# Performance work log

Hardware: AMD Instinct MI355X
Metric: run time of the kernel (lower is better)

The kernel has to match this reference:

```python
import jax, jax.numpy as jnp
import numpy as np

EPS = 1e-5

def gelu(x):
    return jax.nn.gelu(x, approximate=False)

def conv1x1(x, w, b):
    # x: [B,C,H,W], w: [O,C], b: [O]
    return jnp.einsum('bchw,oc->bohw', x, w) + b[None, :, None, None]

def dwconv3(x, w, b):
    # depthwise 3x3, w: [C,1,3,3]
    C = x.shape[1]
    y = jax.lax.conv_general_dilated(x, w, (1, 1), 'SAME',
                                     feature_group_count=C,
                                     dimension_numbers=('NCHW', 'OIHW', 'NCHW'))
    return y + b[None, :, None, None]

def groupnorm(x, g, b):
    # GroupNorm(1, C): normalize over (C,H,W) per sample, per-channel affine
    m = x.mean(axis=(1, 2, 3), keepdims=True)
    v = x.var(axis=(1, 2, 3), keepdims=True)
    xn = (x - m) * jax.lax.rsqrt(v + EPS)
    return xn * g[None, :, None, None] + b[None, :, None, None]

@jax.custom_vjp
def spike(u):
    return (u > 0.0).astype(u.dtype)

def _spike_fwd(u):
    return spike(u), u

def _spike_bwd(u, g):
    # rectangular surrogate gradient of width 0.5 around the threshold
    return (g * (jnp.abs(u) < 0.5).astype(g.dtype),)

spike.defvjp(_spike_fwd, _spike_bwd)

def lif_along(x, tau, vth, axis):
    # leaky-integrate-fire recurrence along `axis` (H or W) treated as time
    xt = jnp.moveaxis(x, axis, 0)  # [T, ...]
    z = jnp.zeros_like(xt[0])
    def step(carry, x_t):
        u_prev, o_prev = carry
        u = x_t + tau * u_prev * (1.0 - o_prev)  # hard reset on spike
        o = spike(u - vth)
        return (u, o), o
    _, out = jax.lax.scan(step, (z, z), xt)
    return jnp.moveaxis(out, 0, axis)


def setup_inputs() -> dict:
    key = jax.random.key(0)
    ks = jax.random.split(key, 8)
    B, C, H, W = 64, 96, 56, 56
    Hd = 4 * C
    def w(k, shape, s=0.02):
        return jax.random.normal(k, shape, jnp.float32) * s
    f32 = jnp.float32
    return dict(
        x=jax.random.normal(ks[0], (B, C, H, W), f32),
        n1g=jnp.ones(C, f32), n1b=jnp.zeros(C, f32),
        c1w=w(ks[1], (C, C)), c1b=jnp.zeros(C, f32),
        g1g=jnp.ones(C, f32), g1b=jnp.zeros(C, f32),
        dww=w(ks[2], (C, 1, 3, 3)), dwb=jnp.zeros(C, f32),
        g2g=jnp.ones(C, f32), g2b=jnp.zeros(C, f32),
        tau1=jnp.array(0.25, f32), vth1=jnp.array(-1.0, f32),
        tau2=jnp.array(0.25, f32), vth2=jnp.array(-1.0, f32),
        c21w=w(ks[3], (C, C)), c21b=jnp.zeros(C, f32),
        c22w=w(ks[4], (C, C)), c22b=jnp.zeros(C, f32),
        g3g=jnp.ones(C, f32), g3b=jnp.zeros(C, f32),
        c3w=w(ks[5], (C, C)), c3b=jnp.zeros(C, f32),
        n2g=jnp.ones(C, f32), n2b=jnp.zeros(C, f32),
        f1w=w(ks[6], (Hd, C)), f1b=jnp.zeros(Hd, f32),
        f2w=w(ks[7], (C, Hd)), f2b=jnp.zeros(C, f32),
    )


def reference(x, n1g, n1b, c1w, c1b, g1g, g1b, dww, dwb, g2g, g2b,
              tau1, vth1, tau2, vth2, c21w, c21b, c22w, c22b,
              g3g, g3b, c3w, c3b, n2g, n2b, f1w, f1b, f2w, f2b):
    shortcut = x
    # LIF module
    h = groupnorm(x, n1g, n1b)                               # block norm1 (MyNorm)
    h = gelu(groupnorm(conv1x1(h, c1w, c1b), g1g, g1b))      # conv1 -> norm1 -> GELU
    h = gelu(groupnorm(dwconv3(h, dww, dwb), g2g, g2b))      # dw1 -> norm2 -> GELU
    x_lr = lif_along(h, tau1, vth1, axis=2)                  # LIF over H
    x_td = lif_along(h, tau2, vth2, axis=3)                  # LIF over W
    h = gelu(conv1x1(x_lr, c21w, c21b)) + gelu(conv1x1(x_td, c22w, c22b))
    h = conv1x1(groupnorm(h, g3g, g3b), c3w, c3b)            # norm3 -> conv3
    x = shortcut + h
    # MLP branch (1x1 convs)
    m = groupnorm(x, n2g, n2b)
    m = conv1x1(gelu(conv1x1(m, f1w, f1b)), f2w, f2b)
    return x + m
```

## Files before the change

kernel.cpp:

```cpp
#include <hip/hip_runtime.h>

#define BB 64
#define CC 96
#define HH 56
#define WW 56
#define HWSZ (HH*WW)
#define CHW (CC*HWSZ)
#define NTOT ((size_t)BB*CHW)
#define S_SPLIT 32
#define CHUNK (CHW/S_SPLIT)
#define HD 384
#define NP 104

typedef float f32x4  __attribute__((ext_vector_type(4)));
typedef float f32x4v __attribute__((ext_vector_type(4)));
typedef short bf16x8 __attribute__((ext_vector_type(8)));
typedef unsigned short u16x4 __attribute__((ext_vector_type(4)));

__device__ __forceinline__ unsigned short f2bf(float f) {
    unsigned int u = __float_as_uint(f);
    u = (u + 0x7FFFu + ((u >> 16) & 1u)) >> 16;
    return (unsigned short)u;
}
__device__ __forceinline__ unsigned int cvtpk(float lo, float hi) {
    unsigned int r;
    asm("v_cvt_pk_bf16_f32 %0, %1, %2" : "=v"(r) : "v"(lo), "v"(hi));
    return r;
}
__device__ __forceinline__ unsigned short cvt1(float x) {
    return (unsigned short)cvtpk(x, x);
}
__device__ __forceinline__ float bf2f(unsigned short u) {
    return __uint_as_float(((unsigned int)u) << 16);
}
__device__ __forceinline__ float gelu_t(float x) {
    float s = x*x;
    float q = __builtin_fmaf(s, 0.102943f, 2.3021953f) * x;
    float t = exp2f(q);
    float r = __builtin_amdgcn_rcpf(1.0f + t);
    return __builtin_fmaf(-x, r, x);
}
__device__ __forceinline__ bf16x8 ldfrag(const unsigned short* p) {
    return *reinterpret_cast<const bf16x8*>(p);
}
template<int NPART>
__device__ __forceinline__ float2 stats_from_parts(const float2* __restrict__ part, int b) {
    int lane = threadIdx.x & 63;
    float s = 0.f, q = 0.f;
    for (int i = lane; i < NPART; i += 64) {
        float2 v = part[b*NPART + i];
        s += v.x; q += v.y;
    }
    #pragma unroll
    for (int off = 32; off > 0; off >>= 1) {
        s += __shfl_down(s, off);
        q += __shfl_down(q, off);
    }
    s = __shfl(s, 0); q = __shfl(q, 0);
    float mean = s / (float)CHW;
    float var  = q / (float)CHW - mean*mean;
    return make_float2(mean, rsqrtf(var + 1e-5f));
}

__global__ __launch_bounds__(256) void wconv(const float* __restrict__ c1w, const float* __restrict__ c21w,
        const float* __restrict__ c22w, const float* __restrict__ c3w,
        const float* __restrict__ f1w, const float* __restrict__ f2w,
        unsigned short* __restrict__ wbf) {
    int i = blockIdx.x*256 + threadIdx.x;
    int blk = i / 9216;
    int idx = i - blk*9216;
    int tm   = idx / 1536;
    int rem  = idx - tm*1536;
    int ks   = rem / 512;
    int rem2 = rem - ks*512;
    int lane = rem2 >> 3;
    int j    = rem2 & 7;
    int row = tm*16 + (lane & 15);
    int col = ks*32 + (lane >> 4)*8 + j;
    float v;
    if      (blk == 0) v = c1w [row*CC + col];
    else if (blk == 1) v = c21w[row*CC + col];
    else if (blk == 2) v = c22w[row*CC + col];
    else if (blk == 3) v = c3w [row*CC + col];
    else if (blk <  8) v = f1w[((blk-4)*CC + row)*CC + col];
    else               v = f2w[row*HD + (blk-8)*CC + col];
    wbf[i] = f2bf(v);
}

__global__ __launch_bounds__(256) void gn_partial(const float* __restrict__ in, float2* __restrict__ part) {
    int b = blockIdx.y, s = blockIdx.x;
    const float4* p = (const float4*)(in + (size_t)b*CHW + (size_t)s*CHUNK);
    float sum = 0.f, sq = 0.f;
    for (int i = threadIdx.x; i < CHUNK/4; i += 256) {
        float4 v = p[i];
        sum += v.x+v.y+v.z+v.w;
        sq  += v.x*v.x+v.y*v.y+v.z*v.z+v.w*v.w;
    }
    #pragma unroll
    for (int off = 32; off > 0; off >>= 1) {
        sum += __shfl_down(sum, off);
        sq  += __shfl_down(sq,  off);
    }
    __shared__ float2 red[4];
    int wid = threadIdx.x >> 6, lane = threadIdx.x & 63;
    if (lane == 0) red[wid] = make_float2(sum, sq);
    __syncthreads();
    if (threadIdx.x == 0) {
        for (int i = 1; i < 4; i++) { sum += red[i].x; sq += red[i].y; }
        part[b*S_SPLIT + s] = make_float2(sum, sq);
    }
}

template<bool IN_BF, bool OUT_RES, int NPART>
__global__ __launch_bounds__(256) void convk(const void* __restrict__ in_,
        const unsigned short* __restrict__ wbf, const float* __restrict__ bias,
        const float2* __restrict__ part_in, const float* __restrict__ gam, const float* __restrict__ bet,
        const float* __restrict__ res, void* __restrict__ out_, float2* __restrict__ part_out) {
    __shared__ unsigned short xs[128][NP];
    __shared__ float af0[CC], bf0[CC], af1[CC], bf1[CC];
    __shared__ float2 red[4];
    int tid = threadIdx.x;
    int b0 = blockIdx.y, b1 = b0 + 32;
    int hw0 = blockIdx.x * 64;
    int lane = tid & 63, wv = tid >> 6;
    int mh = wv >> 1, cg = wv & 1;
    bf16x8 wfr[9];
    {
        const unsigned short* wl = wbf + mh*4608 + lane*8;
        #pragma unroll
        for (int i = 0; i < 9; i++) wfr[i] = ldfrag(wl + i*512);
    }
    float2 st0 = stats_from_parts<NPART>(part_in, b0);
    float2 st1 = stats_from_parts<NPART>(part_in, b1);
    if (tid < CC) {
        float a0 = st0.y * gam[tid];
        af0[tid] = a0; bf0[tid] = __builtin_fmaf(-st0.x, a0, bet[tid]);
        float a1 = st1.y * gam[tid];
        af1[tid] = a1; bf1[tid] = __builtin_fmaf(-st1.x, a1, bet[tid]);
    }
    __syncthreads();
    {
        int colq = (tid & 15) * 4;
        for (int c4 = (tid >> 4)*4; c4 < CC; c4 += 64) {
            float v0[4][4], v1[4][4];
            #pragma unroll
            for (int j = 0; j < 4; j++) {
                int c = c4 + j;
                size_t off0 = (size_t)b0*CHW + (size_t)c*HWSZ + hw0 + colq;
                size_t off1 = (size_t)b1*CHW + (size_t)c*HWSZ + hw0 + colq;
                if (IN_BF) {
                    u16x4 u0 = *reinterpret_cast<const u16x4*>((const unsigned short*)in_ + off0);
                    u16x4 u1 = *reinterpret_cast<const u16x4*>((const unsigned short*)in_ + off1);
                    #pragma unroll
                    for (int jj = 0; jj < 4; jj++) {
                        v0[j][jj] = __builtin_fmaf(bf2f((unsigned short)u0[jj]), af0[c], bf0[c]);
                        v1[j][jj] = __builtin_fmaf(bf2f((unsigned short)u1[jj]), af1[c], bf1[c]);
                    }
                } else {
                    f32x4v f0 = *reinterpret_cast<const f32x4v*>((const float*)in_ + off0);
                    f32x4v f1 = *reinterpret_cast<const f32x4v*>((const float*)in_ + off1);
                    #pragma unroll
                    for (int jj = 0; jj < 4; jj++) {
                        v0[j][jj] = __builtin_fmaf(f0[jj], af0[c], bf0[c]);
                        v1[j][jj] = __builtin_fmaf(f1[jj], af1[c], bf1[c]);
                    }
                }
            }
            #pragma unroll
            for (int jj = 0; jj < 4; jj++) {
                *reinterpret_cast<uint2*>(&xs[colq+jj][c4]) =
                    make_uint2(cvtpk(v0[0][jj],v0[1][jj]), cvtpk(v0[2][jj],v0[3][jj]));
                *reinterpret_cast<uint2*>(&xs[64+colq+jj][c4]) =
                    make_uint2(cvtpk(v1[0][jj],v1[1][jj]), cvtpk(v1[2][jj],v1[3][jj]));
            }
        }
    }
    __syncthreads();
    int ln = lane & 15, k0 = (lane >> 4)*8, r0i = (lane >> 4)*4;
    f32x4 acc[3][4];
    #pragma unroll
    for (int t = 0; t < 3; t++)
        #pragma unroll
        for (int x = 0; x < 4; x++) acc[t][x] = (f32x4){0,0,0,0};
    __builtin_amdgcn_s_setprio(1);
    #pragma unroll
    for (int ks = 0; ks < 3; ks++) {
        bf16x8 bfr[4];
        #pragma unroll
        for (int xr = 0; xr < 4; xr++) bfr[xr] = ldfrag(&xs[cg*64 + xr*16 + ln][ks*32+k0]);
        #pragma unroll
        for (int tm = 0; tm < 3; tm++) {
            #pragma unroll
            for (int xr = 0; xr < 4; xr++)
                acc[tm][xr] = __builtin_amdgcn_mfma_f32_16x16x32_bf16(wfr[tm*3+ks], bfr[xr], acc[tm][xr], 0, 0, 0);
        }
    }
    __builtin_amdgcn_s_setprio(0);
    size_t obase = (size_t)(cg ? b1 : b0)*CHW + hw0;
    float s = 0.f, q = 0.f;
    #pragma unroll
    for (int tm = 0; tm < 3; tm++) {
        #pragma unroll
        for (int xr = 0; xr < 4; xr++) {
            #pragma unroll
            for (int r = 0; r < 4; r++) {
                int o = mh*48 + tm*16 + r0i + r;
                size_t idx = obase + (size_t)o*HWSZ + xr*16 + ln;
                float v = acc[tm][xr][r] + bias[o];
                if (OUT_RES) { v += res[idx]; ((float*)out_)[idx] = v; }
                else         { ((unsigned short*)out_)[idx] = cvt1(v); }
                s += v; q += v*v;
            }
        }
    }
    #pragma unroll
    for (int off = 32; off > 0; off >>= 1) { s += __shfl_down(s, off); q += __shfl_down(q, off); }
    if (lane == 0) red[wv] = make_float2(s, q);
    __syncthreads();
    if (tid == 0) {
        part_out[b0*49 + blockIdx.x] = make_float2(red[0].x + red[2].x, red[0].y + red[2].y);
        part_out[b1*49 + blockIdx.x] = make_float2(red[1].x + red[3].x, red[1].y + red[3].y);
    }
}

__global__ __launch_bounds__(256) void dw_fused(const unsigned short* __restrict__ t1,
        const float* __restrict__ dww, const float* __restrict__ dwb,
        const float2* __restrict__ part_in, const float* __restrict__ gam, const float* __restrict__ bet,
        unsigned short* __restrict__ t2, float2* __restrict__ part_out) {
    __shared__ float tile[HH*57];
    __shared__ float2 red[4];
    int bc = blockIdx.x;
    int b = bc / CC, c = bc - b*CC;
    int tid = threadIdx.x;
    float2 st = stats_from_parts<49>(part_in, b);
    float ga = gam[c]*st.y;
    float bb = __builtin_fmaf(-st.x, ga, bet[c]);
    const unsigned short* ip = t1 + (size_t)bc*HWSZ;
    for (int i = tid; i < HWSZ/4; i += 256) {
        u16x4 v = *reinterpret_cast<const u16x4*>(ip + (size_t)i*4);
        int h = i / 14;
        int w0 = (i - h*14)*4;
        float* tp = &tile[h*57 + w0];
        #pragma unroll
        for (int j = 0; j < 4; j++)
            tp[j] = gelu_t(__builtin_fmaf(bf2f((unsigned short)v[j]), ga, bb));
    }
    __syncthreads();
    float w00=dww[c*9+0],w01=dww[c*9+1],w02=dww[c*9+2],
          w10=dww[c*9+3],w11=dww[c*9+4],w12=dww[c*9+5],
          w20=dww[c*9+6],w21=dww[c*9+7],w22=dww[c*9+8];
    float bs = dwb[c];
    unsigned short* op = t2 + (size_t)bc*HWSZ;
    float s = 0.f, q = 0.f;
    for (int i = tid; i < HWSZ; i += 256) {
        int h = i/WW, w_ = i - h*WW;
        float acc = bs;
        int up = h > 0, dn = h < HH-1, lf = w_ > 0, rt = w_ < WW-1;
        const float* rm = &tile[(h-1)*57 + w_];
        const float* r0p = &tile[h*57 + w_];
        const float* rp = &tile[(h+1)*57 + w_];
        if (up) { if (lf) acc += rm[-1]*w00; acc += rm[0]*w01; if (rt) acc += rm[1]*w02; }
        if (lf) acc += r0p[-1]*w10;
        acc += r0p[0]*w11;
        if (rt) acc += r0p[1]*w12;
        if (dn) { if (lf) acc += rp[-1]*w20; acc += rp[0]*w21; if (rt) acc += rp[1]*w22; }
        op[i] = cvt1(acc);
        s += acc; q += acc*acc;
    }
    #pragma unroll
    for (int off = 32; off > 0; off >>= 1) { s += __shfl_down(s, off); q += __shfl_down(q, off); }
    int wid = tid >> 6, lane = tid & 63;
    if (lane == 0) red[wid] = make_float2(s, q);
    __syncthreads();
    if (tid == 0) {
        for (int i = 1; i < 4; i++) { s += red[i].x; q += red[i].y; }
        part_out[bc] = make_float2(s, q);
    }
}

__global__ __launch_bounds__(64) void lif_hw(const unsigned short* __restrict__ t2,
        unsigned char* __restrict__ xlr, unsigned char* __restrict__ xtd,
        const float2* __restrict__ part_in, const float* __restrict__ gam, const float* __restrict__ bet,
        const float* __restrict__ tau1p, const float* __restrict__ vth1p,
        const float* __restrict__ tau2p, const float* __restrict__ vth2p) {
    __shared__ unsigned short tile[HH*58];
    __shared__ unsigned char spA[HH*60];
    int bc = blockIdx.x;
    int b = bc / CC, c = bc - b*CC;
    int tid = threadIdx.x;
    float2 st = stats_from_parts<96>(part_in, b);
    float ga = gam[c]*st.y;
    float bb = __builtin_fmaf(-st.x, ga, bet[c]);
    const unsigned short* ip = t2 + (size_t)bc*HWSZ;
    for (int i = tid; i < HWSZ/4; i += 64) {
        u16x4 v = *reinterpret_cast<const u16x4*>(ip + i*4);
        int h = i / 14;
        int w0 = (i - h*14)*4;
        unsigned short* tp = &tile[h*58 + w0];
        #pragma unroll
        for (int j = 0; j < 4; j++)
            tp[j] = cvt1(gelu_t(__builtin_fmaf(bf2f((unsigned short)v[j]), ga, bb)));
    }
    __syncthreads();
    const float tau1 = *tau1p, vth1 = *vth1p;
    if (tid < WW) {
        float u = 0.f, o = 0.f;
        for (int h = 0; h < HH; h++) {
            float xv = bf2f(tile[h*58 + tid]);
            u = xv + tau1*u*(1.f - o);
            o = (u - vth1 > 0.f) ? 1.f : 0.f;
            spA[h*60 + tid] = (o != 0.f) ? 1 : 0;
        }
    }
    __syncthreads();
    const float tau2 = *tau2p, vth2 = *vth2p;
    if (tid < HH) {
        float u = 0.f, o = 0.f;
        int off = tid*58;
        for (int w_ = 0; w_ < WW; w_++) {
            float xv = bf2f(tile[off + w_]);
            u = xv + tau2*u*(1.f - o);
            o = (u - vth2 > 0.f) ? 1.f : 0.f;
            tile[off + w_] = (o != 0.f) ? 1 : 0;
        }
    }
    __syncthreads();
    size_t base = (size_t)bc*HWSZ;
    unsigned int* lr32 = (unsigned int*)(xlr + base);
    unsigned int* td32 = (unsigned int*)(xtd + base);
    for (int i = tid; i < HWSZ/4; i += 64) {
        int h = i / 14;
        int w0 = (i - h*14)*4;
        unsigned int a = (unsigned int)spA[h*60+w0] | ((unsigned int)spA[h*60+w0+1]<<8)
                       | ((unsigned int)spA[h*60+w0+2]<<16) | ((unsigned int)spA[h*60+w0+3]<<24);
        unsigned int t = (unsigned int)(tile[h*58+w0]&1) | ((unsigned int)(tile[h*58+w0+1]&1)<<8)
                       | ((unsigned int)(tile[h*58+w0+2]&1)<<16) | ((unsigned int)(tile[h*58+w0+3]&1)<<24);
        lr32[i] = a;
        td32[i] = t;
    }
}

__global__ __launch_bounds__(256) void dual_mfma(const unsigned char* __restrict__ xa_g, const unsigned char* __restrict__ xb_g,
        const unsigned short* __restrict__ w1bf, const float* __restrict__ b1,
        const unsigned short* __restrict__ w2bf, const float* __restrict__ b2,
        unsigned short* __restrict__ out, float2* __restrict__ part_out) {
    __shared__ unsigned short xa[64][NP];
    __shared__ unsigned short xb[64][NP];
    __shared__ float2 red[4];
    int tid = threadIdx.x;
    int b = blockIdx.y;
    int hw0 = blockIdx.x * 64;
    {
        int colq = (tid & 15) * 4;
        const unsigned char* ap = xa_g + (size_t)b*CHW + hw0 + colq;
        const unsigned char* bp = xb_g + (size_t)b*CHW + hw0 + colq;
        for (int c4 = (tid >> 4)*4; c4 < CC; c4 += 64) {
            unsigned int ua[4], ub[4];
            #pragma unroll
            for (int j = 0; j < 4; j++) {
                ua[j] = *reinterpret_cast<const unsigned int*>(ap + (size_t)(c4+j)*HWSZ);
                ub[j] = *reinterpret_cast<const unsigned int*>(bp + (size_t)(c4+j)*HWSZ);
            }
            #pragma unroll
            for (int jj = 0; jj < 4; jj++) {
                unsigned int sh = jj*8;
                unsigned int la = (((ua[0]>>sh)&1u)*0x3F80u) | (((ua[1]>>sh)&1u)*0x3F800000u);
                unsigned int ha = (((ua[2]>>sh)&1u)*0x3F80u) | (((ua[3]>>sh)&1u)*0x3F800000u);
                unsigned int lb = (((ub[0]>>sh)&1u)*0x3F80u) | (((ub[1]>>sh)&1u)*0x3F800000u);
                unsigned int hb = (((ub[2]>>sh)&1u)*0x3F80u) | (((ub[3]>>sh)&1u)*0x3F800000u);
                *reinterpret_cast<uint2*>(&xa[colq+jj][c4]) = make_uint2(la, ha);
                *reinterpret_cast<uint2*>(&xb[colq+jj][c4]) = make_uint2(lb, hb);
            }
        }
    }
    __syncthreads();
    int lane = tid & 63, wv = tid >> 6;
    int mh = wv >> 1, cg = wv & 1;
    int ln = lane & 15, k0 = (lane >> 4)*8, r0i = (lane >> 4)*4;
    const unsigned short* wl1 = w1bf + mh*4608 + lane*8;
    const unsigned short* wl2 = w2bf + mh*4608 + lane*8;
    f32x4 acc1[3][2], acc2[3][2];
    #pragma unroll
    for (int t = 0; t < 3; t++) {
        acc1[t][0] = (f32x4){0,0,0,0}; acc1[t][1] = (f32x4){0,0,0,0};
        acc2[t][0] = (f32x4){0,0,0,0}; acc2[t][1] = (f32x4){0,0,0,0};
    }
    __builtin_amdgcn_s_setprio(1);
    #pragma unroll
    for (int ks = 0; ks < 3; ks++) {
        bf16x8 bfa0 = ldfrag(&xa[cg*32 + ln][ks*32+k0]);
        bf16x8 bfa1 = ldfrag(&xa[cg*32 + 16 + ln][ks*32+k0]);
        bf16x8 bfb0 = ldfrag(&xb[cg*32 + ln][ks*32+k0]);
        bf16x8 bfb1 = ldfrag(&xb[cg*32 + 16 + ln][ks*32+k0]);
        #pragma unroll
        for (int tm = 0; tm < 3; tm++) {
            bf16x8 af1 = ldfrag(wl1 + (tm*3+ks)*512);
            bf16x8 af2 = ldfrag(wl2 + (tm*3+ks)*512);
            acc1[tm][0] = __builtin_amdgcn_mfma_f32_16x16x32_bf16(af1, bfa0, acc1[tm][0], 0, 0, 0);
            acc1[tm][1] = __builtin_amdgcn_mfma_f32_16x16x32_bf16(af1, bfa1, acc1[tm][1], 0, 0, 0);
            acc2[tm][0] = __builtin_amdgcn_mfma_f32_16x16x32_bf16(af2, bfb0, acc2[tm][0], 0, 0, 0);
            acc2[tm][1] = __builtin_amdgcn_mfma_f32_16x16x32_bf16(af2, bfb1, acc2[tm][1], 0, 0, 0);
        }
    }
    __builtin_amdgcn_s_setprio(0);
    size_t ob = (size_t)b*CHW + hw0;
    float s = 0.f, q = 0.f;
    #pragma unroll
    for (int tm = 0; tm < 3; tm++) {
        #pragma unroll
        for (int xr = 0; xr < 2; xr++) {
            #pragma unroll
            for (int r = 0; r < 4; r++) {
                int o = mh*48 + tm*16 + r0i + r;
                float v = gelu_t(acc1[tm][xr][r] + b1[o]) + gelu_t(acc2[tm][xr][r] + b2[o]);
                out[ob + (size_t)o*HWSZ + cg*32 + xr*16 + ln] = cvt1(v);
                s += v; q += v*v;
            }
        }
    }
    #pragma unroll
    for (int off = 32; off > 0; off >>= 1) { s += __shfl_down(s, off); q += __shfl_down(q, off); }
    if (lane == 0) red[wv] = make_float2(s, q);
    __syncthreads();
    if (tid == 0) {
        for (int i = 1; i < 4; i++) { s += red[i].x; q += red[i].y; }
        part_out[b*49 + blockIdx.x] = make_float2(s, q);
    }
}

__global__ __launch_bounds__(256, 6) void mlp_mfma(float* __restrict__ xio, const float2* __restrict__ part_in,
        const float* __restrict__ gam, const float* __restrict__ bet,
        const unsigned short* __restrict__ wbf, const float* __restrict__ b1, const float* __restrict__ b2) {
    __shared__ unsigned short xs[64][NP];
    __shared__ unsigned short mc[64][NP];
    __shared__ float afc[CC], bfc[CC];
    int tid = threadIdx.x;
    int b = blockIdx.y;
    int hw0 = blockIdx.x * 64;
    int lane = tid & 63, wv = tid >> 6;
    int mh = wv >> 1;
    int cg = wv & 1;
    float2 st = stats_from_parts<49>(part_in, b);
    if (tid < CC) {
        float a = st.y * gam[tid];
        afc[tid] = a; bfc[tid] = __builtin_fmaf(-st.x, a, bet[tid]);
    }
    __syncthreads();
    {
        int col = tid & 63;
        size_t base = (size_t)b*CHW + hw0 + col;
        for (int c4 = (tid >> 6)*4; c4 < CC; c4 += 16) {
            float v[4];
            #pragma unroll
            for (int j = 0; j < 4; j++) {
                int c = c4 + j;
                float rv = xio[base + (size_t)c*HWSZ];
                v[j] = __builtin_fmaf(rv, afc[c], bfc[c]);
            }
            *reinterpret_cast<uint2*>(&xs[col][c4]) =
                make_uint2(cvtpk(v[0],v[1]), cvtpk(v[2],v[3]));
        }
    }
    __syncthreads();
    int ln = lane & 15, k0 = (lane >> 4)*8;
    int r0i = (lane >> 4)*4;
    int xrow0 = cg*32 + ln;
    int xrow1 = xrow0 + 16;
    f32x4 ao[3][2];
    #pragma unroll
    for (int t = 0; t < 3; t++) { ao[t][0] = (f32x4){0,0,0,0}; ao[t][1] = (f32x4){0,0,0,0}; }
    for (int ch = 0; ch < 4; ch++) {
        const unsigned short* w1l = wbf + (4+ch)*9216 + mh*4608 + lane*8;
        const unsigned short* w2l = wbf + (8+ch)*9216 + mh*4608 + lane*8;
        f32x4 c1[3][2];
        #pragma unroll
        for (int t = 0; t < 3; t++) { c1[t][0] = (f32x4){0,0,0,0}; c1[t][1] = (f32x4){0,0,0,0}; }
        __builtin_amdgcn_s_setprio(1);
        #pragma unroll
        for (int ks = 0; ks < 3; ks++) {
            bf16x8 bfa = ldfrag(&xs[xrow0][ks*32+k0]);
            bf16x8 bfb = ldfrag(&xs[xrow1][ks*32+k0]);
            #pragma unroll
            for (int tm = 0; tm < 3; tm++) {
                bf16x8 af = ldfrag(w1l + (tm*3+ks)*512);
                c1[tm][0] = __builtin_amdgcn_mfma_f32_16x16x32_bf16(af, bfa, c1[tm][0], 0, 0, 0);
                c1[tm][1] = __builtin_amdgcn_mfma_f32_16x16x32_bf16(af, bfb, c1[tm][1], 0, 0, 0);
            }
        }
        __builtin_amdgcn_s_setprio(0);
        #pragma unroll
        for (int tm = 0; tm < 3; tm++) {
            int d0 = mh*48 + tm*16 + r0i;
            int dch = ch*CC + d0;
            float g0 = gelu_t(c1[tm][0][0] + b1[dch+0]);
            float g1 = gelu_t(c1[tm][0][1] + b1[dch+1]);
            float g2 = gelu_t(c1[tm][0][2] + b1[dch+2]);
            float g3 = gelu_t(c1[tm][0][3] + b1[dch+3]);
            *reinterpret_cast<uint2*>(&mc[xrow0][d0]) = make_uint2(cvtpk(g0,g1), cvtpk(g2,g3));
            float h0 = gelu_t(c1[tm][1][0] + b1[dch+0]);
            float h1 = gelu_t(c1[tm][1][1] + b1[dch+1]);
            float h2 = gelu_t(c1[tm][1][2] + b1[dch+2]);
            float h3 = gelu_t(c1[tm][1][3] + b1[dch+3]);
            *reinterpret_cast<uint2*>(&mc[xrow1][d0]) = make_uint2(cvtpk(h0,h1), cvtpk(h2,h3));
        }
        __syncthreads();
        __builtin_amdgcn_s_setprio(1);
        #pragma unroll
        for (int ks = 0; ks < 3; ks++) {
            bf16x8 bfa = ldfrag(&mc[xrow0][ks*32+k0]);
            bf16x8 bfb = ldfrag(&mc[xrow1][ks*32+k0]);
            #pragma unroll
            for (int tm = 0; tm < 3; tm++) {
                bf16x8 af = ldfrag(w2l + (tm*3+ks)*512);
                ao[tm][0] = __builtin_amdgcn_mfma_f32_16x16x32_bf16(af, bfa, ao[tm][0], 0, 0, 0);
                ao[tm][1] = __builtin_amdgcn_mfma_f32_16x16x32_bf16(af, bfb, ao[tm][1], 0, 0, 0);
            }
        }
        __builtin_amdgcn_s_setprio(0);
        __syncthreads();
    }
    size_t ob = (size_t)b*CHW + hw0 + cg*32 + ln;
    #pragma unroll
    for (int tm = 0; tm < 3; tm++) {
        #pragma unroll
        for (int r = 0; r < 4; r++) {
            int o = mh*48 + tm*16 + r0i + r;
            size_t i0 = ob + (size_t)o*HWSZ;
            float bo = b2[o];
            xio[i0]      = xio[i0]      + bo + ao[tm][0][r];
            xio[i0 + 16] = xio[i0 + 16] + bo + ao[tm][1][r];
        }
    }
}

extern "C" void kernel_launch(void* const* d_in, const int* in_sizes, int n_in,
                              void* d_out, int out_size, void* d_ws, size_t ws_size,
                              hipStream_t stream) {
    (void)in_sizes; (void)n_in; (void)out_size; (void)ws_size;
    const float* x    = (const float*)d_in[0];
    const float* n1g  = (const float*)d_in[1];
    const float* n1b  = (const float*)d_in[2];
    const float* c1w  = (const float*)d_in[3];
    const float* c1b  = (const float*)d_in[4];
    const float* g1g  = (const float*)d_in[5];
    const float* g1b  = (const float*)d_in[6];
    const float* dww  = (const float*)d_in[7];
    const float* dwb  = (const float*)d_in[8];
    const float* g2g  = (const float*)d_in[9];
    const float* g2b  = (const float*)d_in[10];
    const float* tau1 = (const float*)d_in[11];
    const float* vth1 = (const float*)d_in[12];
    const float* tau2 = (const float*)d_in[13];
    const float* vth2 = (const float*)d_in[14];
    const float* c21w = (const float*)d_in[15];
    const float* c21b = (const float*)d_in[16];
    const float* c22w = (const float*)d_in[17];
    const float* c22b = (const float*)d_in[18];
    const float* g3g  = (const float*)d_in[19];
    const float* g3b  = (const float*)d_in[20];
    const float* c3w  = (const float*)d_in[21];
    const float* c3b  = (const float*)d_in[22];
    const float* n2g  = (const float*)d_in[23];
    const float* n2b  = (const float*)d_in[24];
    const float* f1w  = (const float*)d_in[25];
    const float* f1b  = (const float*)d_in[26];
    const float* f2w  = (const float*)d_in[27];
    const float* f2b  = (const float*)d_in[28];
    float* out = (float*)d_out;

    unsigned short* A   = (unsigned short*)d_ws;
    unsigned short* Bb  = A  + NTOT;
    unsigned short* Cc  = Bb + NTOT;
    unsigned short* WBF = Cc + NTOT;
    float2* part0 = (float2*)(WBF + 110592);
    float2* part1 = part0 + 64*32;
    float2* part2 = part1 + 64*49;
    float2* part3 = part2 + 64*96;
    float2* part4 = part3 + 64*49;

    const unsigned short* Wc1  = WBF;
    const unsigned short* Wc21 = WBF + 9216;
    const unsigned short* Wc22 = WBF + 18432;
    const unsigned short* Wc3  = WBF + 27648;

    unsigned char* Au8 = (unsigned char*)A;
    unsigned char* Cu8 = (unsigned char*)Cc;

    dim3 gStat(S_SPLIT, BB);
    dim3 gPair(HWSZ/64, BB/2);
    dim3 gSing(HWSZ/64, BB);

    wconv<<<432,256,0,stream>>>(c1w, c21w, c22w, c3w, f1w, f2w, WBF);
    gn_partial<<<gStat,256,0,stream>>>(x, part0);
    convk<false,false,S_SPLIT><<<gPair,256,0,stream>>>(x, Wc1, c1b, part0, n1g, n1b, nullptr, A, part1);
    dw_fused<<<BB*CC,256,0,stream>>>(A, dww, dwb, part1, g1g, g1b, Bb, part2);
    lif_hw<<<BB*CC,64,0,stream>>>(Bb, Au8, Cu8, part2, g2g, g2b, tau1, vth1, tau2, vth2);
    dual_mfma<<<gSing,256,0,stream>>>(Au8, Cu8, Wc21, c21b, Wc22, c22b, Bb, part3);
    convk<true,true,49><<<gPair,256,0,stream>>>(Bb, Wc3, c3b, part3, g3g, g3b, x, out, part4);
    mlp_mfma<<<gSing,256,0,stream>>>(out, part4, n2g, n2b, WBF, f1b, f2b);
}
```

Measured before the change: 270.6 us.

## Run H and W LIF scans concurrently and pack two planes per block

The LIF kernel now processes two (b,c) planes per 256-thread block. Within each plane, one wavefront runs the H-direction scan while another runs the W-direction scan at the same time, instead of running them one after the other. The W-scan output goes to a separate spike buffer rather than overwriting the input tile. The goal is to shorten the serial recurrence critical path and raise occupancy, at the cost of more shared memory per block.

```diff
diff --git a/kernel.cpp b/kernel.cpp
--- a/kernel.cpp
+++ b/kernel.cpp
@@ -278,63 +278,76 @@
     }
 }
 
-__global__ __launch_bounds__(64) void lif_hw(const unsigned short* __restrict__ t2,
+__global__ __launch_bounds__(256) void lif_hw(const unsigned short* __restrict__ t2,
         unsigned char* __restrict__ xlr, unsigned char* __restrict__ xtd,
         const float2* __restrict__ part_in, const float* __restrict__ gam, const float* __restrict__ bet,
         const float* __restrict__ tau1p, const float* __restrict__ vth1p,
         const float* __restrict__ tau2p, const float* __restrict__ vth2p) {
-    __shared__ unsigned short tile[HH*58];
-    __shared__ unsigned char spA[HH*60];
-    int bc = blockIdx.x;
+    __shared__ unsigned short tile[2][HH*58];
+    __shared__ unsigned char  spA[2][HH*60];
+    __shared__ unsigned char  spB[2][HH*60];
+    int tid = threadIdx.x;
+    int pl = tid >> 7;
+    int lt = tid & 127;
+    int bc = blockIdx.x*2 + pl;
     int b = bc / CC, c = bc - b*CC;
-    int tid = threadIdx.x;
     float2 st = stats_from_parts<96>(part_in, b);
     float ga = gam[c]*st.y;
     float bb = __builtin_fmaf(-st.x, ga, bet[c]);
     const unsigned short* ip = t2 + (size_t)bc*HWSZ;
-    for (int i = tid; i < HWSZ/4; i += 64) {
-        u16x4 v = *reinterpret_cast<const u16x4*>(ip + i*4);
+    for (int i = lt; i < HWSZ/4; i += 128) {
+        u16x4 v = *reinterpret_cast<const u16x4*>(ip + (size_t)i*4);
         int h = i / 14;
         int w0 = (i - h*14)*4;
-        unsigned short* tp = &tile[h*58 + w0];
+        unsigned short* tp = &tile[pl][h*58 + w0];
         #pragma unroll
         for (int j = 0; j < 4; j++)
             tp[j] = cvt1(gelu_t(__builtin_fmaf(bf2f((unsigned short)v[j]), ga, bb)));
     }
     __syncthreads();
-    const float tau1 = *tau1p, vth1 = *vth1p;
-    if (tid < WW) {
-        float u = 0.f, o = 0.f;
-        for (int h = 0; h < HH; h++) {
-            float xv = bf2f(tile[h*58 + tid]);
-            u = xv + tau1*u*(1.f - o);
-            o = (u - vth1 > 0.f) ? 1.f : 0.f;
-            spA[h*60 + tid] = (o != 0.f) ? 1 : 0;
-        }
-    }
-    __syncthreads();
-    const float tau2 = *tau2p, vth2 = *vth2p;
-    if (tid < HH) {
-        float u = 0.f, o = 0.f;
-        int off = tid*58;
-        for (int w_ = 0; w_ < WW; w_++) {
-            float xv = bf2f(tile[off + w_]);
-            u = xv + tau2*u*(1.f - o);
-            o = (u - vth2 > 0.f) ? 1.f : 0.f;
-            tile[off + w_] = (o != 0.f) ? 1 : 0;
+    {
+        int role = (tid >> 6) & 1;
+        int lane = tid & 63;
+        if (role == 0) {
+            const float tau1 = *tau1p, vth1 = *vth1p;
+            if (lane < WW) {
+                float u = 0.f, o = 0.f;
+                #pragma unroll 4
+                for (int h = 0; h < HH; h++) {
+                    float xv = bf2f(tile[pl][h*58 + lane]);
+                    u = xv + tau1*u*(1.f - o);
+                    o = (u - vth1 > 0.f) ? 1.f : 0.f;
+                    spA[pl][h*60 + lane] = (o != 0.f) ? 1 : 0;
+                }
+            }
+        } else {
+            const float tau2 = *tau2p, vth2 = *vth2p;
+            if (lane < HH) {
+                float u = 0.f, o = 0.f;
+                int off = lane*58;
+                #pragma unroll 4
+                for (int w_ = 0; w_ < WW; w_++) {
+                    float xv = bf2f(tile[pl][off + w_]);
+                    u = xv + tau2*u*(1.f - o);
+                    o = (u - vth2 > 0.f) ? 1.f : 0.f;
+                    spB[pl][lane*60 + w_] = (o != 0.f) ? 1 : 0;
+                }
+            }
         }
     }
     __syncthreads();
     size_t base = (size_t)bc*HWSZ;
     unsigned int* lr32 = (unsigned int*)(xlr + base);
     unsigned int* td32 = (unsigned int*)(xtd + base);
-    for (int i = tid; i < HWSZ/4; i += 64) {
+    for (int i = lt; i < HWSZ/4; i += 128) {
         int h = i / 14;
         int w0 = (i - h*14)*4;
-        unsigned int a = (unsigned int)spA[h*60+w0] | ((unsigned int)spA[h*60+w0+1]<<8)
-                       | ((unsigned int)spA[h*60+w0+2]<<16) | ((unsigned int)spA[h*60+w0+3]<<24);
-        unsigned int t = (unsigned int)(tile[h*58+w0]&1) | ((unsigned int)(tile[h*58+w0+1]&1)<<8)
-                       | ((unsigned int)(tile[h*58+w0+2]&1)<<16) | ((unsigned int)(tile[h*58+w0+3]&1)<<24);
+        const unsigned char* pa = &spA[pl][h*60 + w0];
+        const unsigned char* pb = &spB[pl][h*60 + w0];
+        unsigned int a = (unsigned int)pa[0] | ((unsigned int)pa[1]<<8)
+                       | ((unsigned int)pa[2]<<16) | ((unsigned int)pa[3]<<24);
+        unsigned int t = (unsigned int)pb[0] | ((unsigned int)pb[1]<<8)
+                       | ((unsigned int)pb[2]<<16) | ((unsigned int)pb[3]<<24);
         lr32[i] = a;
         td32[i] = t;
     }
@@ -594,7 +607,7 @@
     gn_partial<<<gStat,256,0,stream>>>(x, part0);
     convk<false,false,S_SPLIT><<<gPair,256,0,stream>>>(x, Wc1, c1b, part0, n1g, n1b, nullptr, A, part1);
     dw_fused<<<BB*CC,256,0,stream>>>(A, dww, dwb, part1, g1g, g1b, Bb, part2);
-    lif_hw<<<BB*CC,64,0,stream>>>(Bb, Au8, Cu8, part2, g2g, g2b, tau1, vth1, tau2, vth2);
+    lif_hw<<<BB*CC/2,256,0,stream>>>(Bb, Au8, Cu8, part2, g2g, g2b, tau1, vth1, tau2, vth2);
     dual_mfma<<<gSing,256,0,stream>>>(Au8, Cu8, Wc21, c21b, Wc22, c22b, Bb, part3);
     convk<true,true,49><<<gPair,256,0,stream>>>(Bb, Wc3, c3b, part3, g3g, g3b, x, out, part4);
     mlp_mfma<<<gSing,256,0,stream>>>(out, part4, n2g, n2b, WBF, f1b, f2b);
```

Result: slower. 278.1 us (+2.8%).
